# Optimization experiments

Measured on AMD Instinct MI355X. Metric: run time of the kernel, lower is better.

## Reference

```python
import jax, jax.numpy as jnp
import numpy as np

TEMPERATURE = 0.07


def setup_inputs() -> dict:
    key = jax.random.key(0)
    k1, k2, k3 = jax.random.split(key, 3)
    b, num_proposals, num_phrases, f = 128, 100, 16, 512
    img_features = jax.random.normal(k1, (b, num_proposals, f), dtype=jnp.float32)
    text_features = jax.random.normal(k2, (b, num_phrases, f), dtype=jnp.float32)
    labels = jax.random.randint(k3, (b, b), 0, 2, dtype=jnp.int64)
    return {"img_features": img_features, "text_features": text_features, "labels": labels}


def reference(img_features, text_features, labels):
    # att_matrix[b,d,t,i] = <text[b,t,:], img[d,i,:]>
    att_matrix = jnp.einsum('btf,dif->bdti', text_features, img_features)
    argmax_box = att_matrix.max(axis=3)        # [b, d, t]  max over proposals
    score_matrix = argmax_box.mean(axis=2)     # [b, d]     mean over phrases
    score_exp = jnp.exp(score_matrix / TEMPERATURE)
    return score_exp
```

## Files before the change

### kernel.cpp

```cpp
#include <hip/hip_runtime.h>
#include <hip/hip_bf16.h>
#include <stdint.h>


typedef __attribute__((ext_vector_type(4))) int   v4i;
typedef __attribute__((ext_vector_type(8))) int   v8i;
typedef __attribute__((ext_vector_type(4))) float f32x4;

constexpr int Bb = 128;
constexpr int P  = 100;
constexpr int T  = 16;
constexpr int F  = 512;
constexpr float TEMP = 0.07f;
constexpr int NDPB = 4;

#define GLDS(src, dst) __builtin_amdgcn_global_load_lds( \
    (const __attribute__((address_space(1))) void*)(src), \
    (__attribute__((address_space(3))) void*)(dst), 16, 0, 0)

__global__ void cvt_kernel(const float4* __restrict__ img, const float4* __restrict__ txt,
                           uint32_t* __restrict__ imgb, uint32_t* __restrict__ txtb,
                           int nimg4, int ntxt4) {
  const int stride = gridDim.x * blockDim.x;
  for (int i = blockIdx.x * blockDim.x + threadIdx.x; i < nimg4; i += stride) {
    float4 v = img[i];
    int w = __builtin_amdgcn_cvt_pk_fp8_f32(v.x, v.y, 0, false);
    w     = __builtin_amdgcn_cvt_pk_fp8_f32(v.z, v.w, w, true);
    imgb[i] = (uint32_t)w;
  }
  for (int i = blockIdx.x * blockDim.x + threadIdx.x; i < ntxt4; i += stride) {
    float4 v = txt[i];
    int w = __builtin_amdgcn_cvt_pk_fp8_f32(v.x, v.y, 0, false);
    w     = __builtin_amdgcn_cvt_pk_fp8_f32(v.z, v.w, w, true);
    txtb[i] = (uint32_t)w;
  }
}

__global__ __launch_bounds__(256, 1)
void score_main(const uint8_t* __restrict__ gi, const uint8_t* __restrict__ gt,
                float* __restrict__ out) {
  __shared__ __align__(16) uint8_t As[128 * 512];
  __shared__ __align__(16) uint8_t Bs[2][128 * 256];
  __shared__ float red[NDPB][128][2];

  const int g    = blockIdx.x;
  const int y    = blockIdx.y;
  const int tid  = threadIdx.x;
  const int lane = tid & 63;
  const int w    = tid >> 6;
  const int q    = lane >> 4;
  const int n    = lane & 15;
  const int mh   = w & 1;
  const int nh   = w >> 1;

  {
    const int sub = lane >> 5;
    const int cw  = lane & 31;
    #pragma unroll
    for (int i = 0; i < 16; i++) {
      const int grp = i * 4 + w;
      const int row = grp * 2 + sub;
      const int cg  = cw ^ (row & 7);
      GLDS(gt + (size_t)(y * 128 + row) * F + cg * 16, &As[grp * 1024]);
    }
  }
  auto stageB = [&](int buf, int d, int half) {
    const int sub = lane >> 4;
    const int cw  = lane & 15;
    #pragma unroll
    for (int i = 0; i < 8; i++) {
      const int grp  = i * 4 + w;
      const int row  = grp * 4 + sub;
      const int prow = row < P ? row : 0;
      const int cg   = cw ^ (row & 7);
      GLDS(gi + ((size_t)d * P + prow) * F + half * 256 + cg * 16,
           &Bs[buf][grp * 1024]);
    }
  };
  stageB(0, g * NDPB, 0);

  __syncthreads();

  v8i afr[4][4];
  #pragma unroll
  for (int hk = 0; hk < 4; hk++)
    #pragma unroll
    for (int rt = 0; rt < 4; rt++) {
      const int row = mh * 64 + rt * 16 + n;
      const int c   = hk * 8 + 2 * q;
      v4i lo = *(const v4i*)&As[row * 512 + ((c    ) ^ (n & 7)) * 16];
      v4i hi = *(const v4i*)&As[row * 512 + ((c + 1) ^ (n & 7)) * 16];
      afr[hk][rt] = __builtin_shufflevector(lo, hi, 0, 1, 2, 3, 4, 5, 6, 7);
    }

  f32x4 acc[4][4] = {};

  #pragma unroll
  for (int s = 0; s < 2 * NDPB; s++) {
    if (s) __syncthreads();
    if (s + 1 < 2 * NDPB)
      stageB((s + 1) & 1, g * NDPB + ((s + 1) >> 1), (s + 1) & 1);

    const uint8_t* Bp = Bs[s & 1];
    #pragma unroll
    for (int kk = 0; kk < 2; kk++) {
      const int hk = (s & 1) * 2 + kk;
      v8i bfr[4];
      #pragma unroll
      for (int ct = 0; ct < 4; ct++) {
        const int row = nh * 64 + ct * 16 + n;
        const int c   = kk * 8 + 2 * q;
        v4i lo = *(const v4i*)&Bp[row * 256 + ((c    ) ^ (n & 7)) * 16];
        v4i hi = *(const v4i*)&Bp[row * 256 + ((c + 1) ^ (n & 7)) * 16];
        bfr[ct] = __builtin_shufflevector(lo, hi, 0, 1, 2, 3, 4, 5, 6, 7);
      }
      #pragma unroll
      for (int rt = 0; rt < 4; rt++)
        #pragma unroll
        for (int ct = 0; ct < 4; ct++)
          acc[rt][ct] = __builtin_amdgcn_mfma_scale_f32_16x16x128_f8f6f4(
              afr[hk][rt], bfr[ct], acc[rt][ct], 0, 0, 0, 127, 0, 127);
    }

    if (s & 1) {
      const int dd = s >> 1;
      #pragma unroll
      for (int rt = 0; rt < 4; rt++)
        #pragma unroll
        for (int r = 0; r < 4; r++) {
          float v = -3.0e38f;
          #pragma unroll
          for (int ct = 0; ct < 4; ct++) {
            const bool valid = (nh * 64 + ct * 16 + n) < P;
            v = valid ? fmaxf(v, acc[rt][ct][r]) : v;
          }
          #pragma unroll
          for (int off = 1; off < 16; off <<= 1)
            v = fmaxf(v, __shfl_xor(v, off));
          if (n == 0)
            red[dd][mh * 64 + rt * 16 + q * 4 + r][nh] = v;
        }
      #pragma unroll
      for (int rt = 0; rt < 4; rt++)
        #pragma unroll
        for (int ct = 0; ct < 4; ct++)
          acc[rt][ct] = f32x4{0.f, 0.f, 0.f, 0.f};
    }
  }

  __syncthreads();

  if (tid < NDPB * 8) {
    const int dd = tid >> 3, bl = tid & 7;
    float ssum = 0.f;
    #pragma unroll
    for (int t = 0; t < T; t++) {
      const int r = bl * 16 + t;
      ssum += fmaxf(red[dd][r][0], red[dd][r][1]);
    }
    const float arg = fminf(ssum * (1.0f / (T * TEMP)), 88.0f);
    out[(size_t)(y * 8 + bl) * Bb + (g * NDPB + dd)] = expf(arg);
  }
}

__global__ __launch_bounds__(256)
void score_fallback(const float* __restrict__ gi, const float* __restrict__ gt,
                    float* __restrict__ out) {
  __shared__ __align__(16) unsigned char As[128 * 128];
  __shared__ __align__(16) unsigned char Bs[128 * 128];
  __shared__ float red[128][2];

  const int d = blockIdx.x, b0 = blockIdx.y * 8;
  const int tid = threadIdx.x, lane = tid & 63;
  const int q = lane >> 4, n = lane & 15;
  const int w = tid >> 6, mh = w & 1, nh = w >> 1;

  f32x4 acc[4][4] = {};

  for (int kk = 0; kk < F; kk += 128) {
    #pragma unroll
    for (int s = 0; s < 8; s++) {
      const int slot = s * 256 + tid;
      const int row = slot >> 4, half = slot & 15;
      const int colf = half * 8;
      const int offb = row * 128 + ((half >> 1) ^ (row & 7)) * 16 + (half & 1) * 8;
      float4 v0 = *(const float4*)(gt + (size_t)(b0 * T + row) * F + kk + colf);
      float4 v1 = *(const float4*)(gt + (size_t)(b0 * T + row) * F + kk + colf + 4);
      int w0 = __builtin_amdgcn_cvt_pk_fp8_f32(v0.x, v0.y, 0, false);
      w0     = __builtin_amdgcn_cvt_pk_fp8_f32(v0.z, v0.w, w0, true);
      int w1 = __builtin_amdgcn_cvt_pk_fp8_f32(v1.x, v1.y, 0, false);
      w1     = __builtin_amdgcn_cvt_pk_fp8_f32(v1.z, v1.w, w1, true);
      *(uint2*)&As[offb] = make_uint2((uint32_t)w0, (uint32_t)w1);
      const int prow = row < P ? row : 0;
      float4 u0 = *(const float4*)(gi + ((size_t)d * P + prow) * F + kk + colf);
      float4 u1 = *(const float4*)(gi + ((size_t)d * P + prow) * F + kk + colf + 4);
      int x0 = __builtin_amdgcn_cvt_pk_fp8_f32(u0.x, u0.y, 0, false);
      x0     = __builtin_amdgcn_cvt_pk_fp8_f32(u0.z, u0.w, x0, true);
      int x1 = __builtin_amdgcn_cvt_pk_fp8_f32(u1.x, u1.y, 0, false);
      x1     = __builtin_amdgcn_cvt_pk_fp8_f32(u1.z, u1.w, x1, true);
      *(uint2*)&Bs[offb] = make_uint2((uint32_t)x0, (uint32_t)x1);
    }
    __syncthreads();

    const int s0 = (2 * q) ^ (n & 7);
    v8i a[4], bfr[4];
    #pragma unroll
    for (int rt = 0; rt < 4; rt++) {
      const int off = (mh * 64 + rt * 16 + n) * 128;
      v4i lo = *(const v4i*)&As[off + s0 * 16];
      v4i hi = *(const v4i*)&As[off + (s0 ^ 1) * 16];
      a[rt] = __builtin_shufflevector(lo, hi, 0, 1, 2, 3, 4, 5, 6, 7);
    }
    #pragma unroll
    for (int ct = 0; ct < 4; ct++) {
      const int off = (nh * 64 + ct * 16 + n) * 128;
      v4i lo = *(const v4i*)&Bs[off + s0 * 16];
      v4i hi = *(const v4i*)&Bs[off + (s0 ^ 1) * 16];
      bfr[ct] = __builtin_shufflevector(lo, hi, 0, 1, 2, 3, 4, 5, 6, 7);
    }
    #pragma unroll
    for (int rt = 0; rt < 4; rt++)
      #pragma unroll
      for (int ct = 0; ct < 4; ct++)
        acc[rt][ct] = __builtin_amdgcn_mfma_scale_f32_16x16x128_f8f6f4(
            a[rt], bfr[ct], acc[rt][ct], 0, 0, 0, 127, 0, 127);
    __syncthreads();
  }

  #pragma unroll
  for (int rt = 0; rt < 4; rt++) {
    #pragma unroll
    for (int r = 0; r < 4; r++) {
      float v = -3.0e38f;
      #pragma unroll
      for (int ct = 0; ct < 4; ct++) {
        const bool valid = (nh * 64 + ct * 16 + n) < P;
        v = valid ? fmaxf(v, acc[rt][ct][r]) : v;
      }
      #pragma unroll
      for (int off = 1; off < 16; off <<= 1)
        v = fmaxf(v, __shfl_xor(v, off));
      if (n == 0) red[mh * 64 + rt * 16 + q * 4 + r][nh] = v;
    }
  }
  __syncthreads();

  if (tid < 8) {
    float s = 0.f;
    #pragma unroll
    for (int t = 0; t < T; t++)
      s += fmaxf(red[tid * T + t][0], red[tid * T + t][1]);
    out[(size_t)(b0 + tid) * Bb + d] = expf(fminf(s * (1.0f / (T * TEMP)), 88.0f));
  }
}

extern "C" void kernel_launch(void* const* d_in, const int* in_sizes, int n_in,
                              void* d_out, int out_size, void* d_ws, size_t ws_size,
                              hipStream_t stream) {
  const float* img = (const float*)d_in[0];
  const float* txt = (const float*)d_in[1];
  float* out = (float*)d_out;

  const size_t imgN = (size_t)Bb * P * F;
  const size_t txtN = (size_t)Bb * T * F;
  const size_t need = imgN + txtN;

  if (ws_size >= need) {
    uint8_t* imgb = (uint8_t*)d_ws;
    uint8_t* txtb = imgb + imgN;
    cvt_kernel<<<2048, 256, 0, stream>>>((const float4*)img, (const float4*)txt,
                                         (uint32_t*)imgb, (uint32_t*)txtb,
                                         (int)(imgN / 4), (int)(txtN / 4));
    dim3 grid(Bb / NDPB, 16);
    score_main<<<grid, 256, 0, stream>>>(imgb, txtb, out);
  } else {
    dim3 grid(Bb, 16);
    score_fallback<<<grid, 256, 0, stream>>>(img, txt, out);
  }
}
```

Measured before the change: 113.1 us.

## Replace register-resident A tile kernel with one-proposal-set-per-block, XCD-aware grid

Drops the design where each block kept a 128x512 text tile in registers and processed four image batches with double-buffered staging. Each block now computes one (image batch, 8 text batches) tile, loading both operands in 128-wide K chunks into small shared buffers. It launches 2048 blocks with occupancy 4 and maps block IDs so each XCD handles a contiguous range of image batches for L2 locality. This trades text-tile reuse and load/compute overlap for more parallelism and lower register and LDS pressure, at the cost of four times more text loads and a barrier around every K chunk.

```diff
diff --git a/kernel.cpp b/kernel.cpp
--- a/kernel.cpp
+++ b/kernel.cpp
@@ -12,7 +12,6 @@
 constexpr int T  = 16;
 constexpr int F  = 512;
 constexpr float TEMP = 0.07f;
-constexpr int NDPB = 4;
 
 #define GLDS(src, dst) __builtin_amdgcn_global_load_lds( \
     (const __attribute__((address_space(1))) void*)(src), \
@@ -36,15 +35,20 @@
   }
 }
 
-__global__ __launch_bounds__(256, 1)
-void score_main(const uint8_t* __restrict__ gi, const uint8_t* __restrict__ gt,
-                float* __restrict__ out) {
-  __shared__ __align__(16) uint8_t As[128 * 512];
-  __shared__ __align__(16) uint8_t Bs[2][128 * 256];
-  __shared__ float red[NDPB][128][2];
-
-  const int g    = blockIdx.x;
-  const int y    = blockIdx.y;
+__global__ __launch_bounds__(256, 4)
+void score_kernel(const uint8_t* __restrict__ gi, const uint8_t* __restrict__ gt,
+                  float* __restrict__ out) {
+  __shared__ __align__(16) uint8_t As[128 * 128];
+  __shared__ __align__(16) uint8_t Bs[128 * 128];
+  __shared__ float red[128][2];
+
+  const int id   = blockIdx.x;
+  const int xcd  = id & 7;
+  const int slot = id >> 3;
+  const int d    = xcd * 16 + (slot & 15);
+  const int y    = slot >> 4;
+  const int b0   = y * 8;
+
   const int tid  = threadIdx.x;
   const int lane = tid & 63;
   const int w    = tid >> 6;
@@ -53,65 +57,38 @@
   const int mh   = w & 1;
   const int nh   = w >> 1;
 
-  {
-    const int sub = lane >> 5;
-    const int cw  = lane & 31;
-    #pragma unroll
-    for (int i = 0; i < 16; i++) {
-      const int grp = i * 4 + w;
-      const int row = grp * 2 + sub;
-      const int cg  = cw ^ (row & 7);
-      GLDS(gt + (size_t)(y * 128 + row) * F + cg * 16, &As[grp * 1024]);
-    }
-  }
-  auto stageB = [&](int buf, int d, int half) {
-    const int sub = lane >> 4;
-    const int cw  = lane & 15;
-    #pragma unroll
-    for (int i = 0; i < 8; i++) {
-      const int grp  = i * 4 + w;
-      const int row  = grp * 4 + sub;
-      const int prow = row < P ? row : 0;
-      const int cg   = cw ^ (row & 7);
-      GLDS(gi + ((size_t)d * P + prow) * F + half * 256 + cg * 16,
-           &Bs[buf][grp * 1024]);
-    }
-  };
-  stageB(0, g * NDPB, 0);
-
-  __syncthreads();
-
-  v8i afr[4][4];
-  #pragma unroll
-  for (int hk = 0; hk < 4; hk++)
-    #pragma unroll
-    for (int rt = 0; rt < 4; rt++) {
-      const int row = mh * 64 + rt * 16 + n;
-      const int c   = hk * 8 + 2 * q;
-      v4i lo = *(const v4i*)&As[row * 512 + ((c    ) ^ (n & 7)) * 16];
-      v4i hi = *(const v4i*)&As[row * 512 + ((c + 1) ^ (n & 7)) * 16];
-      afr[hk][rt] = __builtin_shufflevector(lo, hi, 0, 1, 2, 3, 4, 5, 6, 7);
-    }
-
   f32x4 acc[4][4] = {};
 
-  #pragma unroll
-  for (int s = 0; s < 2 * NDPB; s++) {
-    if (s) __syncthreads();
-    if (s + 1 < 2 * NDPB)
-      stageB((s + 1) & 1, g * NDPB + ((s + 1) >> 1), (s + 1) & 1);
-
-    const uint8_t* Bp = Bs[s & 1];
-    #pragma unroll
-    for (int kk = 0; kk < 2; kk++) {
-      const int hk = (s & 1) * 2 + kk;
-      v8i bfr[4];
+  for (int kk = 0; kk < F; kk += 128) {
+    {
+      const int sub = lane >> 3;
+      const int col = (((lane & 7) ^ sub) & 7) * 16;
+      #pragma unroll
+      for (int rr = 0; rr < 4; rr++) {
+        const int c   = rr * 4 + w;
+        const int row = c * 8 + sub;
+        GLDS(gt + (size_t)(b0 * T + row) * F + kk + col, &As[c * 1024]);
+        const int prow = row < P ? row : 0;
+        GLDS(gi + ((size_t)d * P + prow) * F + kk + col, &Bs[c * 1024]);
+      }
+    }
+    __syncthreads();
+
+    {
+      const int s0 = (2 * q) ^ (n & 7);
+      v8i a[4], bfr[4];
+      #pragma unroll
+      for (int rt = 0; rt < 4; rt++) {
+        const int off = (mh * 64 + rt * 16 + n) * 128;
+        v4i lo = *(const v4i*)&As[off + s0 * 16];
+        v4i hi = *(const v4i*)&As[off + (s0 ^ 1) * 16];
+        a[rt] = __builtin_shufflevector(lo, hi, 0, 1, 2, 3, 4, 5, 6, 7);
+      }
       #pragma unroll
       for (int ct = 0; ct < 4; ct++) {
-        const int row = nh * 64 + ct * 16 + n;
-        const int c   = kk * 8 + 2 * q;
-        v4i lo = *(const v4i*)&Bp[row * 256 + ((c    ) ^ (n & 7)) * 16];
-        v4i hi = *(const v4i*)&Bp[row * 256 + ((c + 1) ^ (n & 7)) * 16];
+        const int off = (nh * 64 + ct * 16 + n) * 128;
+        v4i lo = *(const v4i*)&Bs[off + s0 * 16];
+        v4i hi = *(const v4i*)&Bs[off + (s0 ^ 1) * 16];
         bfr[ct] = __builtin_shufflevector(lo, hi, 0, 1, 2, 3, 4, 5, 6, 7);
       }
       #pragma unroll
@@ -119,47 +96,36 @@
         #pragma unroll
         for (int ct = 0; ct < 4; ct++)
           acc[rt][ct] = __builtin_amdgcn_mfma_scale_f32_16x16x128_f8f6f4(
-              afr[hk][rt], bfr[ct], acc[rt][ct], 0, 0, 0, 127, 0, 127);
-    }
-
-    if (s & 1) {
-      const int dd = s >> 1;
-      #pragma unroll
-      for (int rt = 0; rt < 4; rt++)
-        #pragma unroll
-        for (int r = 0; r < 4; r++) {
-          float v = -3.0e38f;
-          #pragma unroll
-          for (int ct = 0; ct < 4; ct++) {
-            const bool valid = (nh * 64 + ct * 16 + n) < P;
-            v = valid ? fmaxf(v, acc[rt][ct][r]) : v;
-          }
-          #pragma unroll
-          for (int off = 1; off < 16; off <<= 1)
-            v = fmaxf(v, __shfl_xor(v, off));
-          if (n == 0)
-            red[dd][mh * 64 + rt * 16 + q * 4 + r][nh] = v;
-        }
-      #pragma unroll
-      for (int rt = 0; rt < 4; rt++)
-        #pragma unroll
-        for (int ct = 0; ct < 4; ct++)
-          acc[rt][ct] = f32x4{0.f, 0.f, 0.f, 0.f};
-    }
-  }
-
+              a[rt], bfr[ct], acc[rt][ct], 0, 0, 0, 127, 0, 127);
+    }
+    __syncthreads();
+  }
+
+  #pragma unroll
+  for (int rt = 0; rt < 4; rt++) {
+    #pragma unroll
+    for (int r = 0; r < 4; r++) {
+      float v = -3.0e38f;
+      #pragma unroll
+      for (int ct = 0; ct < 4; ct++) {
+        const bool valid = (nh * 64 + ct * 16 + n) < P;
+        v = valid ? fmaxf(v, acc[rt][ct][r]) : v;
+      }
+      #pragma unroll
+      for (int off = 1; off < 16; off <<= 1)
+        v = fmaxf(v, __shfl_xor(v, off));
+      if (n == 0)
+        red[mh * 64 + rt * 16 + q * 4 + r][nh] = v;
+    }
+  }
   __syncthreads();
 
-  if (tid < NDPB * 8) {
-    const int dd = tid >> 3, bl = tid & 7;
-    float ssum = 0.f;
-    #pragma unroll
-    for (int t = 0; t < T; t++) {
-      const int r = bl * 16 + t;
-      ssum += fmaxf(red[dd][r][0], red[dd][r][1]);
-    }
-    const float arg = fminf(ssum * (1.0f / (T * TEMP)), 88.0f);
-    out[(size_t)(y * 8 + bl) * Bb + (g * NDPB + dd)] = expf(arg);
+  if (tid < 8) {
+    float s = 0.f;
+    #pragma unroll
+    for (int t = 0; t < T; t++)
+      s += fmaxf(red[tid * T + t][0], red[tid * T + t][1]);
+    out[(size_t)(b0 + tid) * Bb + d] = expf(fminf(s * (1.0f / (T * TEMP)), 88.0f));
   }
 }
 
@@ -271,8 +237,7 @@
     cvt_kernel<<<2048, 256, 0, stream>>>((const float4*)img, (const float4*)txt,
                                          (uint32_t*)imgb, (uint32_t*)txtb,
                                          (int)(imgN / 4), (int)(txtN / 4));
-    dim3 grid(Bb / NDPB, 16);
-    score_main<<<grid, 256, 0, stream>>>(imgb, txtb, out);
+    score_kernel<<<2048, 256, 0, stream>>>(imgb, txtb, out);
   } else {
     dim3 grid(Bb, 16);
     score_fallback<<<grid, 256, 0, stream>>>(img, txt, out);
```

Result: slower. 225.3 us (+99.2%).
